# Kernel tuning notes

Measured on AMD Instinct MI355X. Metric: run time of the kernel, lower is better.

The kernel has to match this reference:

```python
import jax, jax.numpy as jnp
import numpy as np

N = 10000      # nodes
E = 160000     # edges
G = 64         # graphs
NODE_IN = 115
EDGE_IN = 14
H = 256        # hidden
UH = 64        # EdgeUpdate inner hidden
DEPTH = 5
BN_EPS = 1e-5


def setup_inputs() -> dict:
    key = jax.random.key(0)
    ks = jax.random.split(key, 32)
    p = lambda k, shp: (jax.random.normal(k, shp, dtype=jnp.float32) * 0.05)
    inp = {
        "x": jax.random.normal(ks[0], (N, NODE_IN), dtype=jnp.float32),
        "edge_index": jax.random.randint(ks[1], (2, E), 0, N, dtype=jnp.int64) if jax.config.jax_enable_x64 else jax.random.randint(ks[1], (2, E), 0, N).astype(jnp.int32),
        "edge_attr": jax.random.normal(ks[2], (E, EDGE_IN), dtype=jnp.float32),
        "batch": jnp.sort(jax.random.randint(ks[3], (N,), 0, G)).astype(jnp.int32),
        # projections
        "xp_w": p(ks[4], (NODE_IN, H)), "xp_b": jnp.zeros((H,), jnp.float32),
        "ep_w": p(ks[5], (EDGE_IN, H)), "ep_b": jnp.zeros((H,), jnp.float32),
        # EdgeUpdate MLPs (stacked over depth): Linear(3H -> UH) -> ReLU -> Linear(UH -> H)
        "upd_w1": p(ks[6], (DEPTH, 3 * H, UH)), "upd_b1": jnp.zeros((DEPTH, UH), jnp.float32),
        "upd_w2": p(ks[7], (DEPTH, UH, H)),     "upd_b2": jnp.zeros((DEPTH, H), jnp.float32),
        # GINEConv nn MLPs: Linear(H->H) -> ReLU -> Linear(H->H)
        "conv_w1": p(ks[8], (DEPTH, H, H)), "conv_b1": jnp.zeros((DEPTH, H), jnp.float32),
        "conv_w2": p(ks[9], (DEPTH, H, H)), "conv_b2": jnp.zeros((DEPTH, H), jnp.float32),
        # BatchNorm (eval mode: running stats)
        "bn_g": jnp.ones((DEPTH, H), jnp.float32), "bn_b": jnp.zeros((DEPTH, H), jnp.float32),
        "bn_m": jnp.zeros((DEPTH, H), jnp.float32), "bn_v": jnp.ones((DEPTH, H), jnp.float32),
        # readout
        "ro_w": p(ks[10], (H, H)), "ro_b": jnp.zeros((H,), jnp.float32),
    }
    return inp


def reference(x, edge_index, edge_attr, batch, xp_w, xp_b, ep_w, ep_b,
              upd_w1, upd_b1, upd_w2, upd_b2,
              conv_w1, conv_b1, conv_w2, conv_b2,
              bn_g, bn_b, bn_m, bn_v, ro_w, ro_b):
    src, dst = edge_index[0], edge_index[1]
    x = x @ xp_w + xp_b                       # [N, H]
    e = edge_attr @ ep_w + ep_b               # [E, H]
    for i in range(DEPTH):
        # EdgeUpdate: e = e + MLP([x[src], x[dst], e])
        inp = jnp.concatenate([x[src], x[dst], e], axis=-1)          # [E, 3H]
        h = jax.nn.relu(inp @ upd_w1[i] + upd_b1[i])
        e = e + h @ upd_w2[i] + upd_b2[i]
        # GINEConv (eps=0, edge_dim==hidden -> no edge lin):
        # x_new = mlp(x + sum_{(src->dst)} relu(x[src] + e))
        msg = jax.nn.relu(x[src] + e)                                 # [E, H]
        agg = jax.ops.segment_sum(msg, dst, num_segments=N)           # [N, H]
        z = x + agg
        z = jax.nn.relu(z @ conv_w1[i] + conv_b1[i]) @ conv_w2[i] + conv_b2[i]
        # BatchNorm1d (eval: running stats)
        z = (z - bn_m[i]) * jax.lax.rsqrt(bn_v[i] + BN_EPS) * bn_g[i] + bn_b[i]
        x = x + jax.nn.relu(z)
        # dropout is identity in eval mode
    # global_mean_pool over graphs
    counts = jax.ops.segment_sum(jnp.ones((N,), x.dtype), batch, num_segments=G)
    g = jax.ops.segment_sum(x, batch, num_segments=G) / jnp.maximum(counts, 1.0)[:, None]
    return jax.nn.relu(g @ ro_w + ro_b)       # [G, H]
```

## Files before the change

### kernel.cpp

```cpp
#include <hip/hip_runtime.h>

typedef unsigned short ushort_t;
typedef __attribute__((ext_vector_type(4))) float f32x4;
typedef __attribute__((ext_vector_type(8))) short bf16x8;

constexpr int NN = 10000;
constexpr int NE = 160000;
constexpr int NG = 64;
constexpr int NODE_IN_D = 115;
constexpr int EDGE_IN_D = 14;
constexpr int H = 256;
constexpr int UH = 64;
constexpr int DEPTH_D = 5;
constexpr float BN_EPS_F = 1e-5f;

__device__ __forceinline__ float b2fs(ushort_t u) {
  union { unsigned i; float f; } v; v.i = ((unsigned)u) << 16; return v.f;
}
__device__ __forceinline__ ushort_t f2b(float f) {
  union { float f; unsigned i; } v; v.f = f;
  unsigned x = v.i;
  unsigned r = (x + 0x7fffu + ((x >> 16) & 1u)) >> 16;
  return (ushort_t)r;
}

__global__ __launch_bounds__(256) void k_hist(const int* __restrict__ dst,
                                              int* __restrict__ deg)
{
  int j = blockIdx.x * 256 + threadIdx.x;
  if (j < NE) atomicAdd(&deg[dst[j]], 1);
}

__global__ __launch_bounds__(256) void k_scan(const int* __restrict__ deg,
    int* __restrict__ row_ptr, int* __restrict__ cursor)
{
  __shared__ int part[256];
  const int t = threadIdx.x;
  const int base = t * 40;
  int s = 0;
  for (int i = 0; i < 40; ++i) {
    int idx = base + i;
    if (idx < NN) s += deg[idx];
  }
  part[t] = s;
  __syncthreads();
  for (int off = 1; off < 256; off <<= 1) {
    int v = (t >= off) ? part[t - off] : 0;
    __syncthreads();
    part[t] += v;
    __syncthreads();
  }
  int run = (t > 0) ? part[t - 1] : 0;
  for (int i = 0; i < 40; ++i) {
    int idx = base + i;
    if (idx < NN) {
      row_ptr[idx] = run;
      cursor[idx]  = run;
      run += deg[idx];
    }
  }
  if (t == 255) row_ptr[NN] = NE;
}

__global__ __launch_bounds__(256) void k_scatter(const int* __restrict__ src,
    const int* __restrict__ dst, int* __restrict__ cursor,
    int* __restrict__ perm, int* __restrict__ src_p, int* __restrict__ dst_p)
{
  int j = blockIdx.x * 256 + threadIdx.x;
  if (j < NE) {
    int d = dst[j];
    int pos = atomicAdd(&cursor[d], 1);
    perm[pos] = j;
    src_p[pos] = src[j];
    dst_p[pos] = d;
  }
}

__global__ __launch_bounds__(256) void k_proj_edge(const float* __restrict__ ea,
    const int* __restrict__ perm,
    const float* __restrict__ w, const float* __restrict__ b,
    ushort_t* __restrict__ e_p)
{
  __shared__ float as[16][EDGE_IN_D];
  __shared__ int pj[16];
  const int t = threadIdx.x;
  const int row0 = blockIdx.x * 16;
  if (t < 16) pj[t] = perm[row0 + t];
  __syncthreads();
  if (t < 16 * EDGE_IN_D) {
    int r = t / EDGE_IN_D, c = t - r * EDGE_IN_D;
    as[r][c] = ea[(size_t)pj[r] * EDGE_IN_D + c];
  }
  __syncthreads();
  float acc[16];
#pragma unroll
  for (int m = 0; m < 16; ++m) acc[m] = 0.f;
  for (int k = 0; k < EDGE_IN_D; ++k) {
    float wv = w[(size_t)k * H + t];
#pragma unroll
    for (int m = 0; m < 16; ++m) acc[m] += as[m][k] * wv;
  }
  const float bv = b[t];
  for (int m = 0; m < 16; ++m)
    e_p[(size_t)(row0 + m) * H + t] = f2b(acc[m] + bv);
}

__global__ __launch_bounds__(256) void k_pack_all(
    const float* __restrict__ uw1, const float* __restrict__ uw2,
    const float* __restrict__ cw1, const float* __restrict__ cw2,
    const float* __restrict__ xp_w,
    ushort_t* __restrict__ wcP, ushort_t* __restrict__ w2P,
    ushort_t* __restrict__ c1P, ushort_t* __restrict__ c2P,
    ushort_t* __restrict__ pabP, ushort_t* __restrict__ xpP)
{
  int od = blockIdx.x * 256 + threadIdx.x;
  if (od >= DEPTH_D * 24576) {
    int r = od - DEPTH_D * 24576;
    if (r >= 4096) return;
    int lane = r & 63; int nk = r >> 6;
    int ks = nk & 3, nt = nk >> 2;
    int kbase = ks * 32 + (lane >> 4) * 8;
    int n = nt * 16 + (lane & 15);
    ushort_t v[8];
#pragma unroll
    for (int j = 0; j < 8; ++j) {
      int k = kbase + j;
      v[j] = (k < NODE_IN_D) ? f2b(xp_w[(size_t)k * H + n]) : (ushort_t)0;
    }
    uint4 o;
    o.x = (unsigned)v[0] | ((unsigned)v[1] << 16);
    o.y = (unsigned)v[2] | ((unsigned)v[3] << 16);
    o.z = (unsigned)v[4] | ((unsigned)v[5] << 16);
    o.w = (unsigned)v[6] | ((unsigned)v[7] << 16);
    *(uint4*)(xpP + (size_t)r * 8) = o;
    return;
  }
  int depth = od / 24576;
  int r = od - depth * 24576;
  const float* w1d = uw1 + (size_t)depth * 768 * 64;
  const float* W = nullptr; ushort_t* out = nullptr;
  int N = 0, KS = 8; bool pab = false;
  if (r < 2048)       { W = w1d + 512 * 64; out = wcP + (size_t)depth * 2048 * 8; N = 64; KS = 8; }
  else if (r < 4096)  { r -= 2048;  W = uw2 + (size_t)depth * 64 * 256;  out = w2P + (size_t)depth * 2048 * 8; N = 256; KS = 2; }
  else if (r < 12288) { r -= 4096;  W = cw1 + (size_t)depth * 256 * 256; out = c1P + (size_t)depth * 8192 * 8; N = 256; KS = 8; }
  else if (r < 20480) { r -= 12288; W = cw2 + (size_t)depth * 256 * 256; out = c2P + (size_t)depth * 8192 * 8; N = 256; KS = 8; }
  else                { r -= 20480; out = pabP + (size_t)depth * 4096 * 8; N = 128; KS = 8; pab = true; }
  int lane = r & 63; int nk = r >> 6;
  int ks = nk % KS, nt = nk / KS;
  int kbase = ks * 32 + (lane >> 4) * 8;
  int n = nt * 16 + (lane & 15);
  ushort_t v[8];
#pragma unroll
  for (int j = 0; j < 8; ++j) {
    int k = kbase + j;
    float xv;
    if (!pab) xv = W[(size_t)k * N + n];
    else      xv = (n < 64) ? w1d[(size_t)k * 64 + n]
                            : w1d[(size_t)(256 + k) * 64 + (n - 64)];
    v[j] = f2b(xv);
  }
  uint4 o;
  o.x = (unsigned)v[0] | ((unsigned)v[1] << 16);
  o.y = (unsigned)v[2] | ((unsigned)v[3] << 16);
  o.z = (unsigned)v[4] | ((unsigned)v[5] << 16);
  o.w = (unsigned)v[6] | ((unsigned)v[7] << 16);
  *(uint4*)(out + (size_t)r * 8) = o;
}

__global__ __launch_bounds__(256) void k_projm(const float* __restrict__ x,
    const ushort_t* __restrict__ xpP, const float* __restrict__ xpb,
    const ushort_t* __restrict__ pabP0,
    float* __restrict__ xb, float* __restrict__ Pab)
{
  __shared__ __align__(16) ushort_t sa[2 * 32 * 128];
  __shared__ __align__(16) ushort_t sx[2 * 32 * 256];
  const int t = threadIdx.x, l = t & 63, w = t >> 6;
  const int row0 = blockIdx.x * 32;
#pragma unroll
  for (int it = 0; it < 16; ++it) {
    int idx = t + it * 256;
    int row = idx >> 7, c = idx & 127;
    int grow = row0 + row;
    float v = (grow < NN && c < NODE_IN_D) ? x[(size_t)grow * NODE_IN_D + c] : 0.f;
    ushort_t h = f2b(v);
    ushort_t lo = f2b(v - b2fs(h));
    int sch = (row * 16 + ((c >> 3) ^ (row & 7))) * 8 + (c & 7);
    sa[sch] = h; sa[4096 + sch] = lo;
  }
  __syncthreads();
  const int mt = w & 1, ntb = (w >> 1) * 8;
  const int lrow = l & 15, lhi = l >> 4;
  const int arow = mt * 16 + lrow, sw = arow & 7;
  f32x4 acc[8];
#pragma unroll
  for (int n = 0; n < 8; ++n) acc[n] = (f32x4){0.f, 0.f, 0.f, 0.f};
#pragma unroll
  for (int ks = 0; ks < 4; ++ks) {
    int sch = (arow * 16 + ((ks * 4 + lhi) ^ sw)) * 8;
    bf16x8 ah = *(const bf16x8*)&sa[sch];
    bf16x8 al = *(const bf16x8*)&sa[4096 + sch];
#pragma unroll
    for (int n = 0; n < 8; ++n) {
      bf16x8 bb = *(const bf16x8*)(xpP + (size_t)(((ntb + n) * 4 + ks) * 64 + l) * 8);
      acc[n] = __builtin_amdgcn_mfma_f32_16x16x32_bf16(ah, bb, acc[n], 0, 0, 0);
      acc[n] = __builtin_amdgcn_mfma_f32_16x16x32_bf16(al, bb, acc[n], 0, 0, 0);
    }
  }
#pragma unroll
  for (int n = 0; n < 8; ++n) {
    int col = (ntb + n) * 16 + lrow;
    float bv = xpb[col];
#pragma unroll
    for (int r = 0; r < 4; ++r) {
      int row = mt * 16 + lhi * 4 + r;
      int grow = row0 + row;
      float v = acc[n][r] + bv;
      if (grow < NN) xb[(size_t)grow * H + col] = v;
      ushort_t h = f2b(v);
      ushort_t lo = f2b(v - b2fs(h));
      int sch = (row * 32 + ((col >> 3) ^ (row & 7))) * 8 + (col & 7);
      sx[sch] = h; sx[8192 + sch] = lo;
    }
  }
  __syncthreads();
  const int ntb2 = (w >> 1) * 4;
  f32x4 pacc[4];
#pragma unroll
  for (int n = 0; n < 4; ++n) pacc[n] = (f32x4){0.f, 0.f, 0.f, 0.f};
#pragma unroll
  for (int ks = 0; ks < 8; ++ks) {
    int sch = (arow * 32 + ((ks * 4 + lhi) ^ sw)) * 8;
    bf16x8 ah = *(const bf16x8*)&sx[sch];
    bf16x8 al = *(const bf16x8*)&sx[8192 + sch];
#pragma unroll
    for (int n = 0; n < 4; ++n) {
      bf16x8 bb = *(const bf16x8*)(pabP0 + (size_t)(((ntb2 + n) * 8 + ks) * 64 + l) * 8);
      pacc[n] = __builtin_amdgcn_mfma_f32_16x16x32_bf16(ah, bb, pacc[n], 0, 0, 0);
      pacc[n] = __builtin_amdgcn_mfma_f32_16x16x32_bf16(al, bb, pacc[n], 0, 0, 0);
    }
  }
#pragma unroll
  for (int n = 0; n < 4; ++n) {
    int col = (ntb2 + n) * 16 + lrow;
#pragma unroll
    for (int r = 0; r < 4; ++r) {
      int row = mt * 16 + lhi * 4 + r;
      int grow = row0 + row;
      if (grow < NN) Pab[(size_t)grow * 128 + col] = pacc[n][r];
    }
  }
}

__global__ __launch_bounds__(256) void k_edge_mfma(
    const float* __restrict__ Pab,
    const int* __restrict__ src_p, const int* __restrict__ dst_p,
    const ushort_t* __restrict__ wcP, const float* __restrict__ b1,
    const ushort_t* __restrict__ w2P, const float* __restrict__ b2,
    ushort_t* __restrict__ e_p,
    const float* __restrict__ xb, float* __restrict__ agg, int write_e)
{
  __shared__ __align__(16) ushort_t es[64 * 256];
  __shared__ __align__(16) ushort_t hsm[64 * 64];
  __shared__ int sid[64], did[64];
  const int t = threadIdx.x;
  const int l = t & 63;
  const int w = t >> 6;
  const int e0 = blockIdx.x * 64;
  if (t < 64) { sid[t] = src_p[e0 + t]; did[t] = dst_p[e0 + t]; }
#pragma unroll
  for (int it = 0; it < 8; ++it) {
    int idx = t + it * 256;
    int row = idx >> 5, ch = idx & 31;
    uint4 v = *(const uint4*)(e_p + (size_t)(e0 + row) * H + ch * 8);
    *(uint4*)&es[(row * 32 + (ch ^ (row & 7))) * 8] = v;
  }
  __syncthreads();

  const int rw = w * 16;
  const int lrow = l & 15, lhi = l >> 4;

  bf16x8 af[8];
  {
    int arow = rw + lrow;
    int sw = arow & 7;
#pragma unroll
    for (int ks = 0; ks < 8; ++ks)
      af[ks] = *(const bf16x8*)&es[(arow * 32 + ((ks * 4 + lhi) ^ sw)) * 8];
  }
  f32x4 acc[4];
#pragma unroll
  for (int nt = 0; nt < 4; ++nt) {
    f32x4 a = {0.f, 0.f, 0.f, 0.f};
#pragma unroll
    for (int ks = 0; ks < 8; ++ks) {
      bf16x8 bb = *(const bf16x8*)(wcP + (size_t)((nt * 8 + ks) * 64 + l) * 8);
      a = __builtin_amdgcn_mfma_f32_16x16x32_bf16(af[ks], bb, a, 0, 0, 0);
    }
    acc[nt] = a;
  }
#pragma unroll
  for (int nt = 0; nt < 4; ++nt) {
    int col = nt * 16 + lrow;
    float bv = b1[col];
#pragma unroll
    for (int r = 0; r < 4; ++r) {
      int row = rw + lhi * 4 + r;
      float v = acc[nt][r] + Pab[(size_t)sid[row] * 128 + col]
                           + Pab[(size_t)did[row] * 128 + 64 + col] + bv;
      hsm[row * 64 + (col ^ ((row & 7) << 3))] = f2b(fmaxf(v, 0.f));
    }
  }
  __syncthreads();

  bf16x8 ag[2];
  {
    int arow = rw + lrow;
    int sw = arow & 7;
#pragma unroll
    for (int ks = 0; ks < 2; ++ks)
      ag[ks] = *(const bf16x8*)&hsm[arow * 64 + (((ks * 4 + lhi) ^ sw)) * 8];
  }
#pragma unroll
  for (int nt = 0; nt < 16; ++nt) {
    int col = nt * 16 + lrow;
    float bv = b2[col];
    f32x4 a;
#pragma unroll
    for (int r = 0; r < 4; ++r) {
      int row = rw + lhi * 4 + r;
      a[r] = b2fs(es[row * 256 + (col ^ ((row & 7) << 3))]) + bv;
    }
    bf16x8 bb0 = *(const bf16x8*)(w2P + (size_t)((nt * 2 + 0) * 64 + l) * 8);
    bf16x8 bb1 = *(const bf16x8*)(w2P + (size_t)((nt * 2 + 1) * 64 + l) * 8);
    a = __builtin_amdgcn_mfma_f32_16x16x32_bf16(ag[0], bb0, a, 0, 0, 0);
    a = __builtin_amdgcn_mfma_f32_16x16x32_bf16(ag[1], bb1, a, 0, 0, 0);
#pragma unroll
    for (int r = 0; r < 4; ++r) {
      int row = rw + lhi * 4 + r;
      es[row * 256 + (col ^ ((row & 7) << 3))] = f2b(a[r]);
    }
  }
  __syncthreads();

  if (write_e) {
#pragma unroll
    for (int it = 0; it < 8; ++it) {
      int idx = t + it * 256;
      int row = idx >> 5, ch = idx & 31;
      uint4 v = *(const uint4*)&es[(row * 32 + (ch ^ (row & 7))) * 8];
      *(uint4*)(e_p + (size_t)(e0 + row) * H + ch * 8) = v;
    }
  }

  {
    const int c0 = l * 4;
    float4 acc4 = make_float4(0.f, 0.f, 0.f, 0.f);
    int cur = did[rw];
#pragma unroll
    for (int r = 0; r < 16; ++r) {
      int row = rw + r;
      int d = did[row];
      if (d != cur) {
        float* gp = agg + (size_t)cur * H + c0;
        atomicAdd(gp + 0, acc4.x); atomicAdd(gp + 1, acc4.y);
        atomicAdd(gp + 2, acc4.z); atomicAdd(gp + 3, acc4.w);
        acc4 = make_float4(0.f, 0.f, 0.f, 0.f);
        cur = d;
      }
      ushort4 ev = *(const ushort4*)&es[row * 256 + (c0 ^ ((row & 7) << 3))];
      float4 xv = *(const float4*)(xb + (size_t)sid[row] * H + c0);
      acc4.x += fmaxf(xv.x + b2fs(ev.x), 0.f);
      acc4.y += fmaxf(xv.y + b2fs(ev.y), 0.f);
      acc4.z += fmaxf(xv.z + b2fs(ev.z), 0.f);
      acc4.w += fmaxf(xv.w + b2fs(ev.w), 0.f);
    }
    float* gp = agg + (size_t)cur * H + c0;
    atomicAdd(gp + 0, acc4.x); atomicAdd(gp + 1, acc4.y);
    atomicAdd(gp + 2, acc4.z); atomicAdd(gp + 3, acc4.w);
  }
}

__global__ __launch_bounds__(256) void k_convm(
    const float* __restrict__ agg,
    const ushort_t* __restrict__ w1P, const float* __restrict__ b1v,
    const ushort_t* __restrict__ w2P, const float* __restrict__ cb2v,
    const float* __restrict__ bng, const float* __restrict__ bnb,
    const float* __restrict__ bnm, const float* __restrict__ bnv,
    float* __restrict__ xb, int do_pab,
    const ushort_t* __restrict__ pabPn, float* __restrict__ Pab)
{
  __shared__ __align__(16) ushort_t sm[2 * 16 * 256];
  __shared__ __align__(16) ushort_t st1[2 * 16 * 256];
  __shared__ __align__(16) float outs[16 * 256];
  const int t = threadIdx.x, l = t & 63, w = t >> 6;
  const int row0 = blockIdx.x * 16;
#pragma unroll
  for (int it = 0; it < 2; ++it) {
    int idx = t + it * 256;
    int row = idx >> 5, ch = idx & 31;
    int grow = row0 + row;
    float4 p = *(const float4*)(xb + (size_t)grow * H + ch * 8);
    float4 q = *(const float4*)(xb + (size_t)grow * H + ch * 8 + 4);
    float4 g = *(const float4*)(agg + (size_t)grow * H + ch * 8);
    float4 h4 = *(const float4*)(agg + (size_t)grow * H + ch * 8 + 4);
    float v[8] = {p.x + g.x, p.y + g.y, p.z + g.z, p.w + g.w,
                  q.x + h4.x, q.y + h4.y, q.z + h4.z, q.w + h4.w};
    ushort_t h8[8], l8[8];
#pragma unroll
    for (int j = 0; j < 8; ++j) { h8[j] = f2b(v[j]); l8[j] = f2b(v[j] - b2fs(h8[j])); }
    uint4 hh, ll;
    hh.x = (unsigned)h8[0] | ((unsigned)h8[1] << 16);
    hh.y = (unsigned)h8[2] | ((unsigned)h8[3] << 16);
    hh.z = (unsigned)h8[4] | ((unsigned)h8[5] << 16);
    hh.w = (unsigned)h8[6] | ((unsigned)h8[7] << 16);
    ll.x = (unsigned)l8[0] | ((unsigned)l8[1] << 16);
    ll.y = (unsigned)l8[2] | ((unsigned)l8[3] << 16);
    ll.z = (unsigned)l8[4] | ((unsigned)l8[5] << 16);
    ll.w = (unsigned)l8[6] | ((unsigned)l8[7] << 16);
    int sch = (row * 32 + (ch ^ (row & 7))) * 8;
    *(uint4*)&sm[sch] = hh;
    *(uint4*)&sm[4096 + sch] = ll;
  }
  __syncthreads();
  const int lrow = l & 15, lhi = l >> 4;
  const int arow = lrow, sw = arow & 7;
  const int ntb = w * 4;
  f32x4 acc[4];
#pragma unroll
  for (int n = 0; n < 4; ++n) acc[n] = (f32x4){0.f, 0.f, 0.f, 0.f};
#pragma unroll
  for (int ks = 0; ks < 8; ++ks) {
    int sch = (arow * 32 + ((ks * 4 + lhi) ^ sw)) * 8;
    bf16x8 ah = *(const bf16x8*)&sm[sch];
    bf16x8 al = *(const bf16x8*)&sm[4096 + sch];
#pragma unroll
    for (int n = 0; n < 4; ++n) {
      bf16x8 bb = *(const bf16x8*)(w1P + (size_t)(((ntb + n) * 8 + ks) * 64 + l) * 8);
      acc[n] = __builtin_amdgcn_mfma_f32_16x16x32_bf16(ah, bb, acc[n], 0, 0, 0);
      acc[n] = __builtin_amdgcn_mfma_f32_16x16x32_bf16(al, bb, acc[n], 0, 0, 0);
    }
  }
#pragma unroll
  for (int n = 0; n < 4; ++n) {
    int col = (ntb + n) * 16 + lrow;
    float bv = b1v[col];
#pragma unroll
    for (int r = 0; r < 4; ++r) {
      int row = lhi * 4 + r;
      float v = fmaxf(acc[n][r] + bv, 0.f);
      ushort_t h = f2b(v);
      ushort_t lo = f2b(v - b2fs(h));
      int sch = (row * 32 + ((col >> 3) ^ (row & 7))) * 8 + (col & 7);
      st1[sch] = h; st1[4096 + sch] = lo;
    }
  }
  __syncthreads();
  f32x4 acc2[4];
#pragma unroll
  for (int n = 0; n < 4; ++n) acc2[n] = (f32x4){0.f, 0.f, 0.f, 0.f};
#pragma unroll
  for (int ks = 0; ks < 8; ++ks) {
    int sch = (arow * 32 + ((ks * 4 + lhi) ^ sw)) * 8;
    bf16x8 ah = *(const bf16x8*)&st1[sch];
    bf16x8 al = *(const bf16x8*)&st1[4096 + sch];
#pragma unroll
    for (int n = 0; n < 4; ++n) {
      bf16x8 bb = *(const bf16x8*)(w2P + (size_t)(((ntb + n) * 8 + ks) * 64 + l) * 8);
      acc2[n] = __builtin_amdgcn_mfma_f32_16x16x32_bf16(ah, bb, acc2[n], 0, 0, 0);
      acc2[n] = __builtin_amdgcn_mfma_f32_16x16x32_bf16(al, bb, acc2[n], 0, 0, 0);
    }
  }
#pragma unroll
  for (int n = 0; n < 4; ++n) {
    int col = (ntb + n) * 16 + lrow;
    float bv = cb2v[col];
#pragma unroll
    for (int r = 0; r < 4; ++r)
      outs[(lhi * 4 + r) * 256 + col] = acc2[n][r] + bv;
  }
  __syncthreads();
#pragma unroll
  for (int it = 0; it < 4; ++it) {
    int idx = t + it * 256;
    int row = idx >> 6, c4 = idx & 63;
    int grow = row0 + row;
    int c0 = c4 * 4;
    float4 z = *(float4*)&outs[row * 256 + c0];
    float4 g4 = *(const float4*)(bng + c0);
    float4 b4 = *(const float4*)(bnb + c0);
    float4 m4 = *(const float4*)(bnm + c0);
    float4 v4 = *(const float4*)(bnv + c0);
    float4 xv = *(const float4*)(xb + (size_t)grow * H + c0);
    xv.x += fmaxf((z.x - m4.x) * rsqrtf(v4.x + BN_EPS_F) * g4.x + b4.x, 0.f);
    xv.y += fmaxf((z.y - m4.y) * rsqrtf(v4.y + BN_EPS_F) * g4.y + b4.y, 0.f);
    xv.z += fmaxf((z.z - m4.z) * rsqrtf(v4.z + BN_EPS_F) * g4.z + b4.z, 0.f);
    xv.w += fmaxf((z.w - m4.w) * rsqrtf(v4.w + BN_EPS_F) * g4.w + b4.w, 0.f);
    *(float4*)(xb + (size_t)grow * H + c0) = xv;
    if (do_pab) {
      float vv[4] = {xv.x, xv.y, xv.z, xv.w};
      ushort_t h8[4], l8[4];
#pragma unroll
      for (int j = 0; j < 4; ++j) { h8[j] = f2b(vv[j]); l8[j] = f2b(vv[j] - b2fs(h8[j])); }
      ushort4 hh, ll;
      hh.x = h8[0]; hh.y = h8[1]; hh.z = h8[2]; hh.w = h8[3];
      ll.x = l8[0]; ll.y = l8[1]; ll.z = l8[2]; ll.w = l8[3];
      int sch = (row * 32 + ((c0 >> 3) ^ (row & 7))) * 8 + (c0 & 7);
      *(ushort4*)&sm[sch] = hh;
      *(ushort4*)&sm[4096 + sch] = ll;
    }
  }
  if (!do_pab) return;
  __syncthreads();
  const int ntb2 = w * 2;
  f32x4 pacc[2];
#pragma unroll
  for (int n = 0; n < 2; ++n) pacc[n] = (f32x4){0.f, 0.f, 0.f, 0.f};
#pragma unroll
  for (int ks = 0; ks < 8; ++ks) {
    int sch = (arow * 32 + ((ks * 4 + lhi) ^ sw)) * 8;
    bf16x8 ah = *(const bf16x8*)&sm[sch];
    bf16x8 al = *(const bf16x8*)&sm[4096 + sch];
#pragma unroll
    for (int n = 0; n < 2; ++n) {
      bf16x8 bb = *(const bf16x8*)(pabPn + (size_t)(((ntb2 + n) * 8 + ks) * 64 + l) * 8);
      pacc[n] = __builtin_amdgcn_mfma_f32_16x16x32_bf16(ah, bb, pacc[n], 0, 0, 0);
      pacc[n] = __builtin_amdgcn_mfma_f32_16x16x32_bf16(al, bb, pacc[n], 0, 0, 0);
    }
  }
#pragma unroll
  for (int n = 0; n < 2; ++n) {
    int col = (ntb2 + n) * 16 + lrow;
#pragma unroll
    for (int r = 0; r < 4; ++r)
      Pab[(size_t)(row0 + lhi * 4 + r) * 128 + col] = pacc[n][r];
  }
}

__global__ void k_count2(const int* __restrict__ batch, float* __restrict__ gcnt)
{
  int g = threadIdx.x;
  int lo = 0, hi = NN;
  while (lo < hi) { int m = (lo + hi) >> 1; if (batch[m] < g) lo = m + 1; else hi = m; }
  int s = lo;
  lo = 0; hi = NN;
  while (lo < hi) { int m = (lo + hi) >> 1; if (batch[m] <= g) lo = m + 1; else hi = m; }
  gcnt[g] = (float)(lo - s);
}

__global__ __launch_bounds__(256) void k_pool(const float* __restrict__ xb,
    const int* __restrict__ batch, float* __restrict__ gsum)
{
  const int t = threadIdx.x;
  const int row0 = blockIdx.x * 32;
  const int c0 = (t & 63) * 4;
  const int rb = (t >> 6) * 8;
  float4 sum = make_float4(0.f, 0.f, 0.f, 0.f);
  int curg = -1;
#pragma unroll
  for (int j = 0; j < 8; ++j) {
    int row = row0 + rb + j;
    if (row < NN) {
      int g = batch[row];
      if (g != curg) {
        if (curg >= 0) {
          float* gp = gsum + (size_t)curg * H + c0;
          atomicAdd(gp + 0, sum.x); atomicAdd(gp + 1, sum.y);
          atomicAdd(gp + 2, sum.z); atomicAdd(gp + 3, sum.w);
        }
        curg = g;
        sum = make_float4(0.f, 0.f, 0.f, 0.f);
      }
      float4 v = *(const float4*)(xb + (size_t)row * H + c0);
      sum.x += v.x; sum.y += v.y; sum.z += v.z; sum.w += v.w;
    }
  }
  if (curg >= 0) {
    float* gp = gsum + (size_t)curg * H + c0;
    atomicAdd(gp + 0, sum.x); atomicAdd(gp + 1, sum.y);
    atomicAdd(gp + 2, sum.z); atomicAdd(gp + 3, sum.w);
  }
}

__global__ __launch_bounds__(256) void k_readout(const float* __restrict__ gsum,
    const float* __restrict__ gcnt, const float* __restrict__ w,
    const float* __restrict__ b, float* __restrict__ out)
{
  __shared__ float gs[H];
  const int g = blockIdx.x;
  const int t = threadIdx.x;
  float cnt = fmaxf(gcnt[g], 1.0f);
  gs[t] = gsum[(size_t)g * H + t] / cnt;
  __syncthreads();
  float acc = 0.f;
  for (int k = 0; k < H; ++k) acc += gs[k] * w[(size_t)k * H + t];
  out[(size_t)g * H + t] = fmaxf(acc + b[t], 0.f);
}

extern "C" void kernel_launch(void* const* d_in, const int* in_sizes, int n_in,
                              void* d_out, int out_size, void* d_ws, size_t ws_size,
                              hipStream_t stream) {
  (void)in_sizes; (void)n_in; (void)out_size; (void)ws_size;
  const float* x    = (const float*)d_in[0];
  const int*   ei   = (const int*)d_in[1];
  const float* ea   = (const float*)d_in[2];
  const int*   batch= (const int*)d_in[3];
  const float* xp_w = (const float*)d_in[4];
  const float* xp_b = (const float*)d_in[5];
  const float* ep_w = (const float*)d_in[6];
  const float* ep_b = (const float*)d_in[7];
  const float* uw1  = (const float*)d_in[8];
  const float* ub1  = (const float*)d_in[9];
  const float* uw2  = (const float*)d_in[10];
  const float* ub2  = (const float*)d_in[11];
  const float* cw1  = (const float*)d_in[12];
  const float* cb1  = (const float*)d_in[13];
  const float* cw2  = (const float*)d_in[14];
  const float* cb2  = (const float*)d_in[15];
  const float* bng  = (const float*)d_in[16];
  const float* bnb  = (const float*)d_in[17];
  const float* bnm  = (const float*)d_in[18];
  const float* bnv  = (const float*)d_in[19];
  const float* ro_w = (const float*)d_in[20];
  const float* ro_b = (const float*)d_in[21];
  float* out = (float*)d_out;

  char* ws = (char*)d_ws;
  float* xb   = (float*)ws;                  ws += (size_t)NN * H * 4;
  float* agg  = (float*)ws;                  ws += (size_t)NN * H * 4;
  float* Pab  = (float*)ws;                  ws += (size_t)NN * 128 * 4;
  float* gsum = (float*)ws;                  ws += (size_t)NG * H * 4;
  float* gcnt = (float*)ws;                  ws += 256;
  ushort_t* e_p = (ushort_t*)ws;             ws += (size_t)NE * H * 2;
  int* deg    = (int*)ws;                    ws += (size_t)NN * 4;
  int* row_ptr= (int*)ws;                    ws += (size_t)(NN + 8) * 4;
  int* cursor = (int*)ws;                    ws += (size_t)NN * 4;
  int* perm   = (int*)ws;                    ws += (size_t)NE * 4;
  int* src_p  = (int*)ws;                    ws += (size_t)NE * 4;
  int* dst_p  = (int*)ws;                    ws += (size_t)NE * 4;
  ushort_t* wcP = (ushort_t*)ws;             ws += (size_t)DEPTH_D * 2048 * 8 * 2;
  ushort_t* w2P = (ushort_t*)ws;             ws += (size_t)DEPTH_D * 2048 * 8 * 2;
  ushort_t* c1P = (ushort_t*)ws;             ws += (size_t)DEPTH_D * 8192 * 8 * 2;
  ushort_t* c2P = (ushort_t*)ws;             ws += (size_t)DEPTH_D * 8192 * 8 * 2;
  ushort_t* pabP= (ushort_t*)ws;             ws += (size_t)DEPTH_D * 4096 * 8 * 2;
  ushort_t* xpP = (ushort_t*)ws;             ws += (size_t)4096 * 8 * 2;

  const int* src = ei;
  const int* dst = ei + NE;
  const int EB = NE / 256;

  hipMemsetAsync(deg, 0, (size_t)NN * 4, stream);
  k_hist<<<EB, 256, 0, stream>>>(dst, deg);
  k_scan<<<1, 256, 0, stream>>>(deg, row_ptr, cursor);
  k_scatter<<<EB, 256, 0, stream>>>(src, dst, cursor, perm, src_p, dst_p);
  k_pack_all<<<496, 256, 0, stream>>>(uw1, uw2, cw1, cw2, xp_w,
                                      wcP, w2P, c1P, c2P, pabP, xpP);
  k_projm<<<313, 256, 0, stream>>>(x, xpP, xp_b, pabP, xb, Pab);
  k_proj_edge<<<NE / 16, 256, 0, stream>>>(ea, perm, ep_w, ep_b, e_p);

  for (int i = 0; i < DEPTH_D; ++i) {
    hipMemsetAsync(agg, 0, (size_t)NN * H * 4, stream);
    int write_e = (i < DEPTH_D - 1) ? 1 : 0;
    k_edge_mfma<<<NE / 64, 256, 0, stream>>>(
        Pab, src_p, dst_p,
        wcP + (size_t)i * 2048 * 8, ub1 + (size_t)i * UH,
        w2P + (size_t)i * 2048 * 8, ub2 + (size_t)i * H,
        e_p, xb, agg, write_e);
    int do_pab = (i < DEPTH_D - 1) ? 1 : 0;
    k_convm<<<NN / 16, 256, 0, stream>>>(
        agg,
        c1P + (size_t)i * 8192 * 8, cb1 + (size_t)i * H,
        c2P + (size_t)i * 8192 * 8, cb2 + (size_t)i * H,
        bng + (size_t)i * H, bnb + (size_t)i * H,
        bnm + (size_t)i * H, bnv + (size_t)i * H,
        xb, do_pab,
        pabP + (size_t)(i + 1 < DEPTH_D ? i + 1 : 0) * 4096 * 8,
        Pab);
  }

  hipMemsetAsync(gsum, 0, (size_t)NG * H * 4, stream);
  k_count2<<<1, 64, 0, stream>>>(batch, gcnt);
  k_pool<<<(NN + 31) / 32, 256, 0, stream>>>(xb, batch, gsum);
  k_readout<<<NG, 256, 0, stream>>>(gsum, gcnt, ro_w, ro_b, out);
}
```

Measured before the change: 739.2 us.

## Split edge aggregation into separate CSR gather kernel without atomics

Moves the message aggregation out of the edge MLP kernel into a new per-node kernel that walks the dst-sorted CSR ranges and writes agg directly, which removes the memset and the float atomics. In exchange the edge kernel now always writes the updated edge features to global memory, and the new kernel reads them back. This adds E*H bf16 of write and read traffic per layer plus an extra launch, including the last layer where the edge write used to be skipped.

```diff
diff --git a/kernel.cpp b/kernel.cpp
--- a/kernel.cpp
+++ b/kernel.cpp
@@ -256,8 +256,7 @@
     const int* __restrict__ src_p, const int* __restrict__ dst_p,
     const ushort_t* __restrict__ wcP, const float* __restrict__ b1,
     const ushort_t* __restrict__ w2P, const float* __restrict__ b2,
-    ushort_t* __restrict__ e_p,
-    const float* __restrict__ xb, float* __restrict__ agg, int write_e)
+    ushort_t* __restrict__ e_p)
 {
   __shared__ __align__(16) ushort_t es[64 * 256];
   __shared__ __align__(16) ushort_t hsm[64 * 64];
@@ -341,43 +340,34 @@
     }
   }
   __syncthreads();
-
-  if (write_e) {
-#pragma unroll
-    for (int it = 0; it < 8; ++it) {
-      int idx = t + it * 256;
-      int row = idx >> 5, ch = idx & 31;
-      uint4 v = *(const uint4*)&es[(row * 32 + (ch ^ (row & 7))) * 8];
-      *(uint4*)(e_p + (size_t)(e0 + row) * H + ch * 8) = v;
-    }
-  }
-
-  {
-    const int c0 = l * 4;
-    float4 acc4 = make_float4(0.f, 0.f, 0.f, 0.f);
-    int cur = did[rw];
-#pragma unroll
-    for (int r = 0; r < 16; ++r) {
-      int row = rw + r;
-      int d = did[row];
-      if (d != cur) {
-        float* gp = agg + (size_t)cur * H + c0;
-        atomicAdd(gp + 0, acc4.x); atomicAdd(gp + 1, acc4.y);
-        atomicAdd(gp + 2, acc4.z); atomicAdd(gp + 3, acc4.w);
-        acc4 = make_float4(0.f, 0.f, 0.f, 0.f);
-        cur = d;
-      }
-      ushort4 ev = *(const ushort4*)&es[row * 256 + (c0 ^ ((row & 7) << 3))];
-      float4 xv = *(const float4*)(xb + (size_t)sid[row] * H + c0);
-      acc4.x += fmaxf(xv.x + b2fs(ev.x), 0.f);
-      acc4.y += fmaxf(xv.y + b2fs(ev.y), 0.f);
-      acc4.z += fmaxf(xv.z + b2fs(ev.z), 0.f);
-      acc4.w += fmaxf(xv.w + b2fs(ev.w), 0.f);
-    }
-    float* gp = agg + (size_t)cur * H + c0;
-    atomicAdd(gp + 0, acc4.x); atomicAdd(gp + 1, acc4.y);
-    atomicAdd(gp + 2, acc4.z); atomicAdd(gp + 3, acc4.w);
-  }
+#pragma unroll
+  for (int it = 0; it < 8; ++it) {
+    int idx = t + it * 256;
+    int row = idx >> 5, ch = idx & 31;
+    uint4 v = *(const uint4*)&es[(row * 32 + (ch ^ (row & 7))) * 8];
+    *(uint4*)(e_p + (size_t)(e0 + row) * H + ch * 8) = v;
+  }
+}
+
+__global__ __launch_bounds__(256) void k_agg(
+    const ushort_t* __restrict__ e_p, const float* __restrict__ xb,
+    const int* __restrict__ src_p, const int* __restrict__ row_ptr,
+    float* __restrict__ agg)
+{
+  const int t = threadIdx.x;
+  const int n = blockIdx.x * 4 + (t >> 6);
+  const int c0 = (t & 63) * 4;
+  const int beg = row_ptr[n], end = row_ptr[n + 1];
+  float4 acc = make_float4(0.f, 0.f, 0.f, 0.f);
+  for (int j = beg; j < end; ++j) {
+    ushort4 ev = *(const ushort4*)(e_p + (size_t)j * H + c0);
+    const float4 xv = *(const float4*)(xb + (size_t)src_p[j] * H + c0);
+    acc.x += fmaxf(xv.x + b2fs(ev.x), 0.f);
+    acc.y += fmaxf(xv.y + b2fs(ev.y), 0.f);
+    acc.z += fmaxf(xv.z + b2fs(ev.z), 0.f);
+    acc.w += fmaxf(xv.w + b2fs(ev.w), 0.f);
+  }
+  *(float4*)(agg + (size_t)n * H + c0) = acc;
 }
 
 __global__ __launch_bounds__(256) void k_convm(
@@ -658,13 +648,12 @@
   k_proj_edge<<<NE / 16, 256, 0, stream>>>(ea, perm, ep_w, ep_b, e_p);
 
   for (int i = 0; i < DEPTH_D; ++i) {
-    hipMemsetAsync(agg, 0, (size_t)NN * H * 4, stream);
-    int write_e = (i < DEPTH_D - 1) ? 1 : 0;
     k_edge_mfma<<<NE / 64, 256, 0, stream>>>(
         Pab, src_p, dst_p,
         wcP + (size_t)i * 2048 * 8, ub1 + (size_t)i * UH,
         w2P + (size_t)i * 2048 * 8, ub2 + (size_t)i * H,
-        e_p, xb, agg, write_e);
+        e_p);
+    k_agg<<<NN / 4, 256, 0, stream>>>(e_p, xb, src_p, row_ptr, agg);
     int do_pab = (i < DEPTH_D - 1) ? 1 : 0;
     k_convm<<<NN / 16, 256, 0, stream>>>(
         agg,
```

Result: faster. 637.1 us (median of 3 runs) (-13.8%).
